# Kernel optimization log

Measured on AMD Instinct MI355X. Metric: run time of the kernel, lower is better.

## Reference

```python
import jax, jax.numpy as jnp
import numpy as np

N_NODES = 100000
N_EDGES = 1600000
IN_DIM, HID_DIM, OUT_DIM = 512, 128, 64


def gcn_layer(x, rows, cols, vals, W, b):
    # support = x @ W; out[i] = sum_{e: rows[e]==i} vals[e] * support[cols[e]] + b
    support = x @ W                      # [N, d_out]
    msgs = vals[:, None] * support[cols]  # [E, d_out] gather
    agg = jax.ops.segment_sum(msgs, rows, num_segments=N_NODES)  # scatter-add
    return agg + b


def setup_inputs() -> dict:
    key = jax.random.key(0)
    ks = jax.random.split(key, 8)
    x = jax.random.normal(ks[0], (N_NODES, IN_DIM), dtype=jnp.float32)
    edge_rows = jax.random.randint(ks[1], (N_EDGES,), 0, N_NODES, dtype=jnp.int32)
    edge_cols = jax.random.randint(ks[2], (N_EDGES,), 0, N_NODES, dtype=jnp.int32)
    edge_vals = jax.random.uniform(ks[3], (N_EDGES,), dtype=jnp.float32)
    W0 = jax.random.normal(ks[4], (IN_DIM, HID_DIM), dtype=jnp.float32) / np.sqrt(IN_DIM)
    b0 = jnp.zeros((HID_DIM,), dtype=jnp.float32)
    W1 = jax.random.normal(ks[5], (HID_DIM, OUT_DIM), dtype=jnp.float32) / np.sqrt(HID_DIM)
    b1 = jnp.zeros((OUT_DIM,), dtype=jnp.float32)
    return {"x": x, "edge_rows": edge_rows, "edge_cols": edge_cols,
            "edge_vals": edge_vals, "W0": W0, "b0": b0, "W1": W1, "b1": b1}


def reference(x, edge_rows, edge_cols, edge_vals, W0, b0, W1, b1):
    h = gcn_layer(x, edge_rows, edge_cols, edge_vals, W0, b0)  # GCN0
    h = jax.nn.relu(h)                                          # activation0
    # dropout: identity in eval mode
    out = gcn_layer(h, edge_rows, edge_cols, edge_vals, W1, b1)  # GCN1
    return out
```

## Files before the change

kernel.cpp:

```cpp
#include <hip/hip_runtime.h>

#define N_NODES 100000
#define N_EDGES 1600000
#define NBUCK   ((N_NODES + 127) / 128)
#define BCAP    4096

typedef __attribute__((ext_vector_type(8))) short bf16x8;
typedef __attribute__((ext_vector_type(4))) float f32x4;

__device__ __forceinline__ unsigned short f2bf(float f) {
    unsigned int u = __builtin_bit_cast(unsigned int, f);
    u = (u + 0x7FFFu + ((u >> 16) & 1u)) >> 16;
    return (unsigned short)u;
}
__device__ __forceinline__ float bfu2f(unsigned short u) {
    return __builtin_bit_cast(float, (unsigned int)u << 16);
}
__device__ __forceinline__ uint2 packbf4(float4 v) {
    uint2 p;
    p.x = (unsigned int)f2bf(v.x) | ((unsigned int)f2bf(v.y) << 16);
    p.y = (unsigned int)f2bf(v.z) | ((unsigned int)f2bf(v.w) << 16);
    return p;
}

__device__ __forceinline__ void block_barrier() {
    asm volatile("s_waitcnt lgkmcnt(0)" ::: "memory");
    __builtin_amdgcn_sched_barrier(0);
    __builtin_amdgcn_s_barrier();
    __builtin_amdgcn_sched_barrier(0);
}

__global__ __launch_bounds__(256) void prep_kernel(const float* __restrict__ W0,
                                                   const float* __restrict__ W1,
                                                   unsigned short* __restrict__ W0t,
                                                   unsigned short* __restrict__ W1t,
                                                   int* __restrict__ bcursor) {
    const int i = blockIdx.x * 256 + threadIdx.x;
    if (i < 512 * 128) {
        const int k = i / 128, c = i % 128;
        W0t[c * 512 + k] = f2bf(W0[i]);
    }
    const int j = i - 512 * 128;
    if (j >= 0 && j < 128 * 64) {
        const int k = j / 64, c = j % 64;
        W1t[c * 128 + k] = f2bf(W1[j]);
    }
    const int z = i - (512 * 128 + 128 * 64);
    if (z >= 0 && z < NBUCK) bcursor[z] = z * BCAP;
}

__global__ __launch_bounds__(256) void gemm1_kernel(const float* __restrict__ A,
                                                    const unsigned short* __restrict__ Wt,
                                                    unsigned short* __restrict__ C, int N) {
    constexpr int K   = 512;
    constexpr int M   = 128;
    constexpr int LDT = 40;

    __shared__ __align__(16) unsigned short As[2][64 * LDT];
    __shared__ __align__(16) unsigned short Bs[2][M * LDT];

    const int tid  = threadIdx.x;
    const int lane = tid & 63;
    const int wid  = tid >> 6;
    const int wm   = wid >> 1;
    const int wn   = wid & 1;
    const int brow = blockIdx.x * 64;

    const int ar0 = tid >> 3, akq = tid & 7;
    const int ar1 = ar0 + 32;
    const bool v0 = (brow + ar0) < N;
    const bool v1 = (brow + ar1) < N;
    const float* ap0 = A + (size_t)(brow + ar0) * K + akq * 4;
    const float* ap1 = A + (size_t)(brow + ar1) * K + akq * 4;
    const int br0 = tid >> 2, bkq = tid & 3;
    const unsigned short* bp0 = Wt + (size_t)br0 * K + bkq * 8;
    const unsigned short* bp1 = Wt + (size_t)(br0 + 64) * K + bkq * 8;

    float4 A0a, A0b, A1a, A1b, A2a, A2b, A3a, A3b;
    uint4  B0a, B0b, B1a, B1b, B2a, B2b, B3a, B3b;

#define ISSUE(s, t) do {                                                          \
        const int ko = (t) * 32;                                                  \
        A##s##a = v0 ? *reinterpret_cast<const float4*>(ap0 + ko)                 \
                     : make_float4(0.f, 0.f, 0.f, 0.f);                           \
        A##s##b = v1 ? *reinterpret_cast<const float4*>(ap1 + ko)                 \
                     : make_float4(0.f, 0.f, 0.f, 0.f);                           \
        B##s##a = *reinterpret_cast<const uint4*>(bp0 + ko);                      \
        B##s##b = *reinterpret_cast<const uint4*>(bp1 + ko);                      \
    } while (0)

#define WLDS(s, buf) do {                                                         \
        *reinterpret_cast<uint2*>(&As[buf][ar0 * LDT + akq * 4]) = packbf4(A##s##a); \
        *reinterpret_cast<uint2*>(&As[buf][ar1 * LDT + akq * 4]) = packbf4(A##s##b); \
        *reinterpret_cast<uint4*>(&Bs[buf][br0 * LDT + bkq * 8]) = B##s##a;          \
        *reinterpret_cast<uint4*>(&Bs[buf][(br0 + 64) * LDT + bkq * 8]) = B##s##b;   \
    } while (0)

    f32x4 acc[2][4];
#pragma unroll
    for (int m = 0; m < 2; ++m)
#pragma unroll
        for (int n = 0; n < 4; ++n) acc[m][n] = (f32x4){0.f, 0.f, 0.f, 0.f};

    const int afo = (wm * 32 + (lane & 15)) * LDT + (lane >> 4) * 8;
    const int bfo = (wn * 64 + (lane & 15)) * LDT + (lane >> 4) * 8;

    auto step = [&](int buf) {
        bf16x8 af[2], bfr[4];
#pragma unroll
        for (int m = 0; m < 2; ++m)
            af[m] = *reinterpret_cast<const bf16x8*>(&As[buf][afo + m * 16 * LDT]);
#pragma unroll
        for (int n = 0; n < 4; ++n)
            bfr[n] = *reinterpret_cast<const bf16x8*>(&Bs[buf][bfo + n * 16 * LDT]);
#pragma unroll
        for (int m = 0; m < 2; ++m)
#pragma unroll
            for (int n = 0; n < 4; ++n)
                acc[m][n] = __builtin_amdgcn_mfma_f32_16x16x32_bf16(af[m], bfr[n], acc[m][n], 0, 0, 0);
    };

    ISSUE(0, 0); ISSUE(1, 1); ISSUE(2, 2); ISSUE(3, 3);
    WLDS(0, 0);
    block_barrier();

#pragma unroll
    for (int i = 0; i < 4; ++i) {
        const int t = 4 * i;
        if (t + 4 < 16) ISSUE(0, t + 4);
        step(0);
        WLDS(1, 1);
        block_barrier();
        if (t + 5 < 16) ISSUE(1, t + 5);
        step(1);
        WLDS(2, 0);
        block_barrier();
        if (t + 6 < 16) ISSUE(2, t + 6);
        step(0);
        WLDS(3, 1);
        block_barrier();
        if (t + 7 < 16) ISSUE(3, t + 7);
        step(1);
        if (t + 4 < 16) WLDS(0, 0);
        block_barrier();
    }
#undef ISSUE
#undef WLDS

    const int rb = brow + wm * 32 + ((lane >> 4) * 4);
    const int cb = wn * 64 + (lane & 15);
#pragma unroll
    for (int m = 0; m < 2; ++m)
#pragma unroll
        for (int n = 0; n < 4; ++n)
#pragma unroll
            for (int j = 0; j < 4; ++j) {
                const int r = rb + m * 16 + j;
                if (r < N) C[(size_t)r * M + cb + n * 16] = f2bf(acc[m][n][j]);
            }
}

#define SCAT_CH 4096
__global__ __launch_bounds__(256) void scatter_bucket_kernel(const int* __restrict__ rows,
                                                             const int* __restrict__ cols,
                                                             const float* __restrict__ vals,
                                                             int* __restrict__ bcursor,
                                                             int2* __restrict__ tmp) {
    __shared__ int hist[NBUCK];
    const int tid = threadIdx.x;
    const int e0  = blockIdx.x * SCAT_CH;

    int   er[16];
    int   ec[16];
    float ev[16];
#pragma unroll
    for (int i = 0; i < 16; ++i) {
        const int e = e0 + i * 256 + tid;
        const bool ok = e < N_EDGES;
        er[i] = ok ? rows[e] : -1;
        ec[i] = ok ? cols[e] : 0;
        ev[i] = ok ? vals[e] : 0.f;
    }

    for (int b = tid; b < NBUCK; b += 256) hist[b] = 0;
    __syncthreads();

#pragma unroll
    for (int i = 0; i < 16; ++i)
        if (er[i] >= 0) atomicAdd(&hist[er[i] >> 7], 1);
    __syncthreads();

    for (int b = tid; b < NBUCK; b += 256) {
        const int hcnt = hist[b];
        hist[b] = (hcnt > 0) ? atomicAdd(&bcursor[b], hcnt) : 0;
    }
    __syncthreads();

#pragma unroll
    for (int i = 0; i < 16; ++i) {
        if (er[i] >= 0) {
            const int pos = atomicAdd(&hist[er[i] >> 7], 1);
            tmp[pos] = make_int2(ec[i] | ((er[i] & 127) << 17), __float_as_int(ev[i]));
        }
    }
}

__global__ __launch_bounds__(512) void spmm_gcn0_kernel(const int* __restrict__ bcursor,
                                                        const int2* __restrict__ tmp,
                                                        const unsigned short* __restrict__ sup,
                                                        const float* __restrict__ bias,
                                                        const unsigned short* __restrict__ W1t,
                                                        unsigned short* __restrict__ sup1) {
    constexpr int DIM = 128;
    constexpr int GL  = 16;
    constexpr int NG  = 4;

    __shared__ int2 eds[BCAP];
    __shared__ int  cnt_sh[128];
    __shared__ int  startsh[128];
    __shared__ int  cur[128];

    const int b    = blockIdx.x;
    const int tid  = threadIdx.x;
    const int base = b * BCAP;
    const int cnt  = bcursor[b] - base;

    int2 w[8];
#pragma unroll
    for (int i = 0; i < 8; ++i) {
        const int j = i * 512 + tid;
        w[i] = (j < cnt) ? tmp[base + j] : make_int2(-1, 0);
    }
    if (tid < 128) cnt_sh[tid] = 0;
    __syncthreads();
#pragma unroll
    for (int i = 0; i < 8; ++i)
        if (w[i].x >= 0) atomicAdd(&cnt_sh[((unsigned int)w[i].x) >> 17], 1);
    __syncthreads();

    if (tid == 0) {
        int a = 0;
        for (int i = 0; i < 128; ++i) { startsh[i] = a; a += cnt_sh[i]; }
    }
    __syncthreads();
    if (tid < 128) cur[tid] = startsh[tid];
    __syncthreads();

#pragma unroll
    for (int i = 0; i < 8; ++i) {
        if (w[i].x >= 0) {
            const int rl  = ((unsigned int)w[i].x) >> 17;
            const int pos = atomicAdd(&cur[rl], 1);
            eds[pos] = make_int2(w[i].x & 0x1FFFF, w[i].y);
        }
    }
    __syncthreads();

    const int lane = tid & 63;
    const int wid  = tid >> 6;
    const int khi  = lane >> 4;
    const int rlo  = lane & 15;
    const int grp  = khi;
    const int sub  = rlo;

    const float4 bb0 = *reinterpret_cast<const float4*>(bias + sub * 8);
    const float4 bb1 = *reinterpret_cast<const float4*>(bias + sub * 8 + 4);

    bf16x8 afr[4];

    for (int r8 = 0; r8 < 16; ++r8) {
        const int rl    = wid * 16 + r8;
        const int start = startsh[rl];
        const int end   = start + cnt_sh[rl];

        float a[8] = {0.f, 0.f, 0.f, 0.f, 0.f, 0.f, 0.f, 0.f};

        int j = start + grp;
        while (j + NG < end) {
            const int2 e0 = eds[j];
            const int2 e1 = eds[j + NG];
            const bf16x8 s0 = *reinterpret_cast<const bf16x8*>(sup + (size_t)e0.x * DIM + sub * 8);
            const bf16x8 s1 = *reinterpret_cast<const bf16x8*>(sup + (size_t)e1.x * DIM + sub * 8);
            const float v0 = __int_as_float(e0.y);
            const float v1 = __int_as_float(e1.y);
#pragma unroll
            for (int d = 0; d < 8; ++d) a[d] = fmaf(v0, bfu2f((unsigned short)s0[d]), a[d]);
#pragma unroll
            for (int d = 0; d < 8; ++d) a[d] = fmaf(v1, bfu2f((unsigned short)s1[d]), a[d]);
            j += 2 * NG;
        }
        for (; j < end; j += NG) {
            const int2 e = eds[j];
            const bf16x8 s = *reinterpret_cast<const bf16x8*>(sup + (size_t)e.x * DIM + sub * 8);
            const float v = __int_as_float(e.y);
#pragma unroll
            for (int d = 0; d < 8; ++d) a[d] = fmaf(v, bfu2f((unsigned short)s[d]), a[d]);
        }

#pragma unroll
        for (int d = 0; d < 8; ++d) {
            a[d] += __shfl_xor(a[d], 16);
            a[d] += __shfl_xor(a[d], 32);
        }

        bf16x8 pk;
        pk[0] = (short)f2bf(fmaxf(a[0] + bb0.x, 0.f));
        pk[1] = (short)f2bf(fmaxf(a[1] + bb0.y, 0.f));
        pk[2] = (short)f2bf(fmaxf(a[2] + bb0.z, 0.f));
        pk[3] = (short)f2bf(fmaxf(a[3] + bb0.w, 0.f));
        pk[4] = (short)f2bf(fmaxf(a[4] + bb1.x, 0.f));
        pk[5] = (short)f2bf(fmaxf(a[5] + bb1.y, 0.f));
        pk[6] = (short)f2bf(fmaxf(a[6] + bb1.z, 0.f));
        pk[7] = (short)f2bf(fmaxf(a[7] + bb1.w, 0.f));
        const uint4 pu = __builtin_bit_cast(uint4, pk);

#pragma unroll
        for (int t = 0; t < 4; ++t) {
            const int src = t * 4 + khi;
            uint4 g;
            g.x = (unsigned int)__shfl((int)pu.x, src);
            g.y = (unsigned int)__shfl((int)pu.y, src);
            g.z = (unsigned int)__shfl((int)pu.z, src);
            g.w = (unsigned int)__shfl((int)pu.w, src);
            if (rlo == r8) afr[t] = __builtin_bit_cast(bf16x8, g);
        }
    }

    const unsigned short* wp = W1t + (size_t)rlo * 128 + khi * 8;
    bf16x8 bf_[4][4];
#pragma unroll
    for (int n = 0; n < 4; ++n)
#pragma unroll
        for (int t = 0; t < 4; ++t)
            bf_[n][t] = *reinterpret_cast<const bf16x8*>(wp + (size_t)n * 16 * 128 + t * 32);

    f32x4 acc2[4];
#pragma unroll
    for (int n = 0; n < 4; ++n) acc2[n] = (f32x4){0.f, 0.f, 0.f, 0.f};
#pragma unroll
    for (int t = 0; t < 4; ++t)
#pragma unroll
        for (int n = 0; n < 4; ++n)
            acc2[n] = __builtin_amdgcn_mfma_f32_16x16x32_bf16(afr[t], bf_[n][t], acc2[n], 0, 0, 0);

    const int rb2 = (b << 7) + wid * 16 + khi * 4;
#pragma unroll
    for (int n = 0; n < 4; ++n)
#pragma unroll
        for (int j = 0; j < 4; ++j) {
            const int r = rb2 + j;
            if (r < N_NODES) sup1[(size_t)r * 64 + n * 16 + rlo] = f2bf(acc2[n][j]);
        }
}

__global__ __launch_bounds__(512) void spmm_bucket64_kernel(const int* __restrict__ bcursor,
                                                            const int2* __restrict__ tmp,
                                                            const unsigned short* __restrict__ sup,
                                                            const float* __restrict__ bias,
                                                            float* __restrict__ outg) {
    constexpr int DIM = 64;
    constexpr int GL  = 8;
    constexpr int NG  = 8;

    __shared__ int2 eds[BCAP];
    __shared__ int  cnt_sh[128];
    __shared__ int  startsh[128];
    __shared__ int  cur[128];

    const int b    = blockIdx.x;
    const int tid  = threadIdx.x;
    const int base = b * BCAP;
    const int cnt  = bcursor[b] - base;

    int2 w[8];
#pragma unroll
    for (int i = 0; i < 8; ++i) {
        const int j = i * 512 + tid;
        w[i] = (j < cnt) ? tmp[base + j] : make_int2(-1, 0);
    }
    if (tid < 128) cnt_sh[tid] = 0;
    __syncthreads();
#pragma unroll
    for (int i = 0; i < 8; ++i)
        if (w[i].x >= 0) atomicAdd(&cnt_sh[((unsigned int)w[i].x) >> 17], 1);
    __syncthreads();

    if (tid == 0) {
        int a = 0;
        for (int i = 0; i < 128; ++i) { startsh[i] = a; a += cnt_sh[i]; }
    }
    __syncthreads();
    if (tid < 128) cur[tid] = startsh[tid];
    __syncthreads();

#pragma unroll
    for (int i = 0; i < 8; ++i) {
        if (w[i].x >= 0) {
            const int rl  = ((unsigned int)w[i].x) >> 17;
            const int pos = atomicAdd(&cur[rl], 1);
            eds[pos] = make_int2(w[i].x & 0x1FFFF, w[i].y);
        }
    }
    __syncthreads();

    const int lane = tid & 63;
    const int wid  = tid >> 6;
    const int grp  = lane / GL;
    const int sub  = lane % GL;

    for (int r8 = 0; r8 < 16; ++r8) {
        const int rl  = wid * 16 + r8;
        const int row = (b << 7) + rl;
        const int start = startsh[rl];
        const int end   = start + cnt_sh[rl];

        float a[8] = {0.f, 0.f, 0.f, 0.f, 0.f, 0.f, 0.f, 0.f};

        int j = start + grp;
        while (j + NG < end) {
            const int2 e0 = eds[j];
            const int2 e1 = eds[j + NG];
            const bf16x8 s0 = *reinterpret_cast<const bf16x8*>(sup + (size_t)e0.x * DIM + sub * 8);
            const bf16x8 s1 = *reinterpret_cast<const bf16x8*>(sup + (size_t)e1.x * DIM + sub * 8);
            const float v0 = __int_as_float(e0.y);
            const float v1 = __int_as_float(e1.y);
#pragma unroll
            for (int d = 0; d < 8; ++d) a[d] = fmaf(v0, bfu2f((unsigned short)s0[d]), a[d]);
#pragma unroll
            for (int d = 0; d < 8; ++d) a[d] = fmaf(v1, bfu2f((unsigned short)s1[d]), a[d]);
            j += 2 * NG;
        }
        for (; j < end; j += NG) {
            const int2 e = eds[j];
            const bf16x8 s = *reinterpret_cast<const bf16x8*>(sup + (size_t)e.x * DIM + sub * 8);
            const float v = __int_as_float(e.y);
#pragma unroll
            for (int d = 0; d < 8; ++d) a[d] = fmaf(v, bfu2f((unsigned short)s[d]), a[d]);
        }

#pragma unroll
        for (int d = 0; d < 8; ++d) {
            a[d] += __shfl_xor(a[d], 8);
            a[d] += __shfl_xor(a[d], 16);
            a[d] += __shfl_xor(a[d], 32);
        }

        if (lane < GL && row < N_NODES) {
            const float4 b0 = *reinterpret_cast<const float4*>(bias + sub * 8);
            const float4 b1 = *reinterpret_cast<const float4*>(bias + sub * 8 + 4);
            float* dst = outg + (size_t)row * DIM + sub * 8;
            *reinterpret_cast<float4*>(dst)     = make_float4(a[0] + b0.x, a[1] + b0.y, a[2] + b0.z, a[3] + b0.w);
            *reinterpret_cast<float4*>(dst + 4) = make_float4(a[4] + b1.x, a[5] + b1.y, a[6] + b1.z, a[7] + b1.w);
        }
    }
}

extern "C" void kernel_launch(void* const* d_in, const int* in_sizes, int n_in,
                              void* d_out, int out_size, void* d_ws, size_t ws_size,
                              hipStream_t stream) {
    const float* x    = (const float*)d_in[0];
    const int*   rows = (const int*)d_in[1];
    const int*   cols = (const int*)d_in[2];
    const float* vals = (const float*)d_in[3];
    const float* W0   = (const float*)d_in[4];
    const float* b0   = (const float*)d_in[5];
    const float* W1   = (const float*)d_in[6];
    const float* b1   = (const float*)d_in[7];
    float*       out  = (float*)d_out;

    char* p = (char*)d_ws;
    unsigned short* sup0 = (unsigned short*)p;  p += (size_t)N_NODES * 128 * 2;
    unsigned short* sup1 = (unsigned short*)p;  p += (size_t)N_NODES * 64 * 2;
    unsigned short* W0t  = (unsigned short*)p;  p += (size_t)512 * 128 * 2;
    unsigned short* W1t  = (unsigned short*)p;  p += (size_t)128 * 64 * 2;
    int*   bcursor  = (int*)p;                  p += (size_t)((NBUCK + 3) / 4) * 16;
    int2*  tmp      = (int2*)p;                 p += (size_t)NBUCK * BCAP * 8;

    const int prep_blocks = (512 * 128 + 128 * 64 + NBUCK + 255) / 256;
    const int scat_blocks = (N_EDGES + SCAT_CH - 1) / SCAT_CH;
    const int gemm_blocks = (N_NODES + 63) / 64;

    prep_kernel<<<prep_blocks, 256, 0, stream>>>(W0, W1, W0t, W1t, bcursor);

    scatter_bucket_kernel<<<scat_blocks, 256, 0, stream>>>(rows, cols, vals, bcursor, tmp);

    gemm1_kernel<<<gemm_blocks, 256, 0, stream>>>(x, W0t, sup0, N_NODES);

    spmm_gcn0_kernel<<<NBUCK, 512, 0, stream>>>(bcursor, tmp, sup0, b0, W1t, sup1);

    spmm_bucket64_kernel<<<NBUCK, 512, 0, stream>>>(bcursor, tmp, sup1, b1, out);
}
```

Baseline: 220.3 us.

## Merge edge scatter and first GEMM into one heterogeneous launch

```diff
diff --git a/kernel.cpp b/kernel.cpp
--- a/kernel.cpp
+++ b/kernel.cpp
@@ -4,6 +4,9 @@
 #define N_EDGES 1600000
 #define NBUCK   ((N_NODES + 127) / 128)
 #define BCAP    4096
+#define SCAT_CH 4096
+#define SCAT_BLOCKS ((N_EDGES + SCAT_CH - 1) / SCAT_CH)
+#define GEMM_BLOCKS ((N_NODES + 63) / 64)
 
 typedef __attribute__((ext_vector_type(8))) short bf16x8;
 typedef __attribute__((ext_vector_type(4))) float f32x4;
@@ -49,22 +52,68 @@
     if (z >= 0 && z < NBUCK) bcursor[z] = z * BCAP;
 }
 
-__global__ __launch_bounds__(256) void gemm1_kernel(const float* __restrict__ A,
-                                                    const unsigned short* __restrict__ Wt,
-                                                    unsigned short* __restrict__ C, int N) {
+__device__ __forceinline__ void scatter_body(int bid, char* smem,
+                                             const int* __restrict__ rows,
+                                             const int* __restrict__ cols,
+                                             const float* __restrict__ vals,
+                                             int* __restrict__ bcursor,
+                                             int2* __restrict__ tmp) {
+    int* hist = (int*)smem;
+    const int tid = threadIdx.x;
+    const int e0  = bid * SCAT_CH;
+
+    int   er[16];
+    int   ec[16];
+    float ev[16];
+#pragma unroll
+    for (int i = 0; i < 16; ++i) {
+        const int e = e0 + i * 256 + tid;
+        const bool ok = e < N_EDGES;
+        er[i] = ok ? rows[e] : -1;
+        ec[i] = ok ? cols[e] : 0;
+        ev[i] = ok ? vals[e] : 0.f;
+    }
+
+    for (int b = tid; b < NBUCK; b += 256) hist[b] = 0;
+    __syncthreads();
+
+#pragma unroll
+    for (int i = 0; i < 16; ++i)
+        if (er[i] >= 0) atomicAdd(&hist[er[i] >> 7], 1);
+    __syncthreads();
+
+    for (int b = tid; b < NBUCK; b += 256) {
+        const int hcnt = hist[b];
+        hist[b] = (hcnt > 0) ? atomicAdd(&bcursor[b], hcnt) : 0;
+    }
+    __syncthreads();
+
+#pragma unroll
+    for (int i = 0; i < 16; ++i) {
+        if (er[i] >= 0) {
+            const int pos = atomicAdd(&hist[er[i] >> 7], 1);
+            tmp[pos] = make_int2(ec[i] | ((er[i] & 127) << 17), __float_as_int(ev[i]));
+        }
+    }
+}
+
+__device__ __forceinline__ void gemm1_body(int bid, char* smem,
+                                           const float* __restrict__ A,
+                                           const unsigned short* __restrict__ Wt,
+                                           unsigned short* __restrict__ C, int N) {
     constexpr int K   = 512;
     constexpr int M   = 128;
     constexpr int LDT = 40;
 
-    __shared__ __align__(16) unsigned short As[2][64 * LDT];
-    __shared__ __align__(16) unsigned short Bs[2][M * LDT];
+    unsigned short* As0 = (unsigned short*)smem;
+    unsigned short* Bs0 = (unsigned short*)(smem + 10240);
 
     const int tid  = threadIdx.x;
     const int lane = tid & 63;
     const int wid  = tid >> 6;
     const int wm   = wid >> 1;
     const int wn   = wid & 1;
-    const int brow = blockIdx.x * 64;
+    const int brow = bid * 64;
 
     const int ar0 = tid >> 3, akq = tid & 7;
     const int ar1 = ar0 + 32;
@@ -89,11 +138,11 @@
         B##s##b = *reinterpret_cast<const uint4*>(bp1 + ko);                      \
     } while (0)
 
-#define WLDS(s, buf) do {                                                         \
-        *reinterpret_cast<uint2*>(&As[buf][ar0 * LDT + akq * 4]) = packbf4(A##s##a); \
-        *reinterpret_cast<uint2*>(&As[buf][ar1 * LDT + akq * 4]) = packbf4(A##s##b); \
-        *reinterpret_cast<uint4*>(&Bs[buf][br0 * LDT + bkq * 8]) = B##s##a;          \
-        *reinterpret_cast<uint4*>(&Bs[buf][(br0 + 64) * LDT + bkq * 8]) = B##s##b;   \
+#define WLDS(s, buf) do {                                                                       \
+        *reinterpret_cast<uint2*>(&As0[(buf) * 2560 + ar0 * LDT + akq * 4]) = packbf4(A##s##a); \
+        *reinterpret_cast<uint2*>(&As0[(buf) * 2560 + ar1 * LDT + akq * 4]) = packbf4(A##s##b); \
+        *reinterpret_cast<uint4*>(&Bs0[(buf) * 5120 + br0 * LDT + bkq * 8]) = B##s##a;          \
+        *reinterpret_cast<uint4*>(&Bs0[(buf) * 5120 + (br0 + 64) * LDT + bkq * 8]) = B##s##b;   \
     } while (0)
 
     f32x4 acc[2][4];
@@ -109,10 +158,10 @@
         bf16x8 af[2], bfr[4];
 #pragma unroll
         for (int m = 0; m < 2; ++m)
-            af[m] = *reinterpret_cast<const bf16x8*>(&As[buf][afo + m * 16 * LDT]);
+            af[m] = *reinterpret_cast<const bf16x8*>(&As0[buf * 2560 + afo + m * 16 * LDT]);
 #pragma unroll
         for (int n = 0; n < 4; ++n)
-            bfr[n] = *reinterpret_cast<const bf16x8*>(&Bs[buf][bfo + n * 16 * LDT]);
+            bfr[n] = *reinterpret_cast<const bf16x8*>(&Bs0[buf * 5120 + bfo + n * 16 * LDT]);
 #pragma unroll
         for (int m = 0; m < 2; ++m)
 #pragma unroll
@@ -160,49 +209,19 @@
             }
 }
 
-#define SCAT_CH 4096
-__global__ __launch_bounds__(256) void scatter_bucket_kernel(const int* __restrict__ rows,
-                                                             const int* __restrict__ cols,
-                                                             const float* __restrict__ vals,
-                                                             int* __restrict__ bcursor,
-                                                             int2* __restrict__ tmp) {
-    __shared__ int hist[NBUCK];
-    const int tid = threadIdx.x;
-    const int e0  = blockIdx.x * SCAT_CH;
-
-    int   er[16];
-    int   ec[16];
-    float ev[16];
-#pragma unroll
-    for (int i = 0; i < 16; ++i) {
-        const int e = e0 + i * 256 + tid;
-        const bool ok = e < N_EDGES;
-        er[i] = ok ? rows[e] : -1;
-        ec[i] = ok ? cols[e] : 0;
-        ev[i] = ok ? vals[e] : 0.f;
-    }
-
-    for (int b = tid; b < NBUCK; b += 256) hist[b] = 0;
-    __syncthreads();
-
-#pragma unroll
-    for (int i = 0; i < 16; ++i)
-        if (er[i] >= 0) atomicAdd(&hist[er[i] >> 7], 1);
-    __syncthreads();
-
-    for (int b = tid; b < NBUCK; b += 256) {
-        const int hcnt = hist[b];
-        hist[b] = (hcnt > 0) ? atomicAdd(&bcursor[b], hcnt) : 0;
-    }
-    __syncthreads();
-
-#pragma unroll
-    for (int i = 0; i < 16; ++i) {
-        if (er[i] >= 0) {
-            const int pos = atomicAdd(&hist[er[i] >> 7], 1);
-            tmp[pos] = make_int2(ec[i] | ((er[i] & 127) << 17), __float_as_int(ev[i]));
-        }
-    }
+__global__ __launch_bounds__(256) void stage1_kernel(const int* __restrict__ rows,
+                                                     const int* __restrict__ cols,
+                                                     const float* __restrict__ vals,
+                                                     int* __restrict__ bcursor,
+                                                     int2* __restrict__ tmp,
+                                                     const float* __restrict__ A,
+                                                     const unsigned short* __restrict__ W0t,
+                                                     unsigned short* __restrict__ sup0) {
+    __shared__ __align__(16) char smem[30720];
+    if (blockIdx.x < SCAT_BLOCKS)
+        scatter_body(blockIdx.x, smem, rows, cols, vals, bcursor, tmp);
+    else
+        gemm1_body(blockIdx.x - SCAT_BLOCKS, smem, A, W0t, sup0, N_NODES);
 }
 
 __global__ __launch_bounds__(512) void spmm_gcn0_kernel(const int* __restrict__ bcursor,
@@ -212,7 +231,6 @@
                                                         const unsigned short* __restrict__ W1t,
                                                         unsigned short* __restrict__ sup1) {
     constexpr int DIM = 128;
-    constexpr int GL  = 16;
     constexpr int NG  = 4;
 
     __shared__ int2 eds[BCAP];
@@ -477,14 +495,11 @@
     int2*  tmp      = (int2*)p;                 p += (size_t)NBUCK * BCAP * 8;
 
     const int prep_blocks = (512 * 128 + 128 * 64 + NBUCK + 255) / 256;
-    const int scat_blocks = (N_EDGES + SCAT_CH - 1) / SCAT_CH;
-    const int gemm_blocks = (N_NODES + 63) / 64;
 
     prep_kernel<<<prep_blocks, 256, 0, stream>>>(W0, W1, W0t, W1t, bcursor);
 
-    scatter_bucket_kernel<<<scat_blocks, 256, 0, stream>>>(rows, cols, vals, bcursor, tmp);
-
-    gemm1_kernel<<<gemm_blocks, 256, 0, stream>>>(x, W0t, sup0, N_NODES);
+    stage1_kernel<<<SCAT_BLOCKS + GEMM_BLOCKS, 256, 0, stream>>>(
+        rows, cols, vals, bcursor, tmp, x, W0t, sup0);
 
     spmm_gcn0_kernel<<<NBUCK, 512, 0, stream>>>(bcursor, tmp, sup0, b0, W1t, sup1);
 
```

Measured after the change: 213.3 us. 1.03x faster.
